# Kernel tuning notes

Measured on AMD Instinct MI355X. Metric: run time of the kernel, lower is better.

The kernel has to match this reference:

```python
import jax, jax.numpy as jnp
import numpy as np

B, T, D = 8, 2048, 256  # batch, time segments, feature dim (a_dim=v_dim=hidden=out=256)
EPS = 1e-8


def _layer_norm(x, g, b, eps=1e-6):
    m = jnp.mean(x, axis=-1, keepdims=True)
    v = jnp.var(x, axis=-1, keepdims=True)
    return (x - m) * jax.lax.rsqrt(v + eps) * g + b


def setup_inputs() -> dict:
    key = jax.random.key(0)
    ks = jax.random.split(key, 9)
    xav = lambda k: jax.random.uniform(k, (D, D), jnp.float32, -1.0, 1.0) * np.sqrt(6.0 / (D + D))
    return {
        "a_fea": jax.random.normal(ks[0], (B, T, D), jnp.float32),
        "v_fea": jax.random.normal(ks[1], (B, T, D), jnp.float32),
        "thr_val": jnp.float32(0.099),
        "Wv1": xav(ks[2]), "Wv2": xav(ks[3]), "Wvfc": xav(ks[4]),
        "Wa1": xav(ks[5]), "Wa2": xav(ks[6]), "Wafc": xav(ks[7]),
        "ln_g": jnp.ones((D,), jnp.float32),
        "ln_b": jnp.zeros((D,), jnp.float32),
    }


def reference(a_fea, v_fea, thr_val, Wv1, Wv2, Wvfc, Wa1, Wa2, Wafc, ln_g, ln_b):
    relu = jax.nn.relu
    # branch projections (dropout is identity at eval); torch Linear: x @ W.T
    v1 = relu(jnp.einsum('btd,hd->bth', v_fea, Wv1))
    v2 = relu(jnp.einsum('btd,hd->bth', v_fea, Wv2))
    a1 = relu(jnp.einsum('btd,hd->bth', a_fea, Wa1))
    a2 = relu(jnp.einsum('btd,hd->bth', a_fea, Wa2))

    d = v2.shape[-1]
    # scaled cross-modal scores, ReLU'd  [B, Tv, Ta]
    beta_va = relu(jnp.einsum('btd,bsd->bts', v2, a1) / jnp.sqrt(jnp.float32(d)))
    # a->v scores taken BEFORE row-normalization of beta_va (as in torch code)
    beta_av = jnp.transpose(beta_va, (0, 2, 1))

    time = beta_va.shape[-1]
    thr = thr_val * 10.0 / time

    # normalize -> threshold sparsify -> renormalize (v attends to a)
    bn_va = beta_va / (jnp.sum(beta_va, axis=-1, keepdims=True) + EPS)
    g_va = jnp.where(bn_va > thr, bn_va, 0.0)
    g_va = g_va / (jnp.sum(g_va, axis=-1, keepdims=True) + EPS)

    # same for a attends to v
    bn_av = beta_av / (jnp.sum(beta_av, axis=-1, keepdims=True) + EPS)
    g_av = jnp.where(bn_av > thr, bn_av, 0.0)
    g_av = g_av / (jnp.sum(g_av, axis=-1, keepdims=True) + EPS)

    # vectorized form of the diagonal selection double-loop (batch element 0)
    pred = (jnp.diagonal(g_av[0]) > 0).astype(jnp.float32)  # [T]

    a_pos = jnp.einsum('bts,bsd->btd', g_va, a2)
    v_psp = v_fea + a_pos
    v_pos = jnp.einsum('bts,bsd->btd', g_av, v1)
    a_psp = a_fea + v_pos

    v_psp = _layer_norm(relu(jnp.einsum('btd,od->bto', v_psp, Wvfc)), ln_g, ln_b)
    a_psp = _layer_norm(relu(jnp.einsum('btd,od->bto', a_psp, Wafc)), ln_g, ln_b)
    a_v_fuse = 0.5 * (v_psp + a_psp)
    return a_v_fuse, v_psp, a_psp, pred
```

## Files before the change

### kernel.cpp

```cpp
#include <hip/hip_runtime.h>
#include <math.h>

#define TT 2048
#define DD 256
#define NBATCH 8
#define EPSF 1e-8f

typedef unsigned short u16;
typedef __attribute__((ext_vector_type(8))) short short8;
typedef __attribute__((ext_vector_type(4))) float f32x4;

__device__ __forceinline__ u16 f2bf(float x) {
    unsigned int u = __builtin_bit_cast(unsigned int, x);
    u += 0x7fffu + ((u >> 16) & 1u);
    return (u16)(u >> 16);
}
__device__ __forceinline__ float bf2f(u16 h) {
    return __builtin_bit_cast(float, (unsigned int)h << 16);
}

__device__ __forceinline__ int frag_dst(int row, int k) {
    return (((row >> 4) * 4 + (k >> 3)) * 16 + (row & 15)) * 8 + (k & 7);
}

__device__ __forceinline__ int swz(int i) { return i ^ ((i >> 2) & 32); }

template<int BR>
__device__ __forceinline__ void stage_tile(const u16* __restrict__ g, u16* s,
                                           int row0, int k0, int ldk, int tid)
{
    #pragma unroll
    for (int i = 0; i < BR / 64; ++i) {
        const int c = tid + 256 * i;
        const int row = c >> 2, q = c & 3;
        *(int4*)(s + swz(frag_dst(row, q * 8))) =
            *(const int4*)(g + (long)(row0 + row) * ldk + k0 + q * 8);
    }
}

__global__ __launch_bounds__(512)
void proj_kernel(const u16* __restrict__ vfh, const u16* __restrict__ vfl,
                 const u16* __restrict__ afh, const u16* __restrict__ afl,
                 const u16* __restrict__ Wsp,
                 u16* __restrict__ v2h, u16* __restrict__ v2l,
                 u16* __restrict__ a1h, u16* __restrict__ a1l,
                 u16* __restrict__ v1T, u16* __restrict__ a2T)
{
    const int zz = blockIdx.z;
    const u16* Ah = (zz == 1 || zz == 3) ? afh : vfh;
    const u16* Al = (zz == 1 || zz == 3) ? afl : vfl;
    const int widx = (zz == 0) ? 2 : (zz == 1) ? 4 : (zz == 2) ? 0 : 6;
    const u16* Bh = Wsp + widx * DD * DD;
    const u16* Bl = Bh + DD * DD;
    const bool split = zz < 2;
    u16* Oh = (zz == 0) ? v2h : a1h;
    u16* Ol = (zz == 0) ? v2l : a1l;
    u16* OT = (zz == 2) ? v1T : a2T;

    __shared__ __align__(16) u16 Ah_s[128 * 32], Al_s[128 * 32];
    __shared__ __align__(16) u16 Bh_s[64 * 32], Bl_s[64 * 32];
    const int m0 = blockIdx.y * 128, n0 = blockIdx.x * 64;
    const int tid = threadIdx.x, lane = tid & 63, w = tid >> 6;
    const int wy = w >> 2, wx = w & 3;
    f32x4 acc[4] = {};

    const int prow = tid >> 2, pq = tid & 3;
    const int dA = swz(frag_dst(prow, pq * 8));
    const u16* gAh = Ah + (long)(m0 + prow) * DD + pq * 8;
    const u16* gAl = Al + (long)(m0 + prow) * DD + pq * 8;
    const int brow = (tid & 255) >> 2, bq = tid & 3;
    const int dB = swz(frag_dst(brow, bq * 8));
    const u16* gB = ((tid < 256) ? Bh : Bl) + (long)(n0 + brow) * DD + bq * 8;
    u16* sB = (tid < 256) ? Bh_s : Bl_s;

    int4 rAh = *(const int4*)(gAh);
    int4 rAl = *(const int4*)(gAl);
    int4 rB  = *(const int4*)(gB);

    for (int k0 = 0; k0 < DD; k0 += 32) {
        *(int4*)(Ah_s + dA) = rAh;
        *(int4*)(Al_s + dA) = rAl;
        *(int4*)(sB + dB)   = rB;
        __syncthreads();
        const int kn = (k0 + 32 < DD) ? k0 + 32 : 0;
        rAh = *(const int4*)(gAh + kn);
        rAl = *(const int4*)(gAl + kn);
        rB  = *(const int4*)(gB + kn);
        short8 ah[4], al[4], bh, bl;
        #pragma unroll
        for (int i = 0; i < 4; ++i) {
            ah[i] = *(const short8*)(Ah_s + swz(((wy * 4 + i) * 64 + lane) * 8));
            al[i] = *(const short8*)(Al_s + swz(((wy * 4 + i) * 64 + lane) * 8));
        }
        bh = *(const short8*)(Bh_s + swz((wx * 64 + lane) * 8));
        bl = *(const short8*)(Bl_s + swz((wx * 64 + lane) * 8));
        #pragma unroll
        for (int i = 0; i < 4; ++i) {
            acc[i] = __builtin_amdgcn_mfma_f32_16x16x32_bf16(ah[i], bl, acc[i], 0, 0, 0);
            acc[i] = __builtin_amdgcn_mfma_f32_16x16x32_bf16(al[i], bh, acc[i], 0, 0, 0);
            acc[i] = __builtin_amdgcn_mfma_f32_16x16x32_bf16(ah[i], bh, acc[i], 0, 0, 0);
        }
        __syncthreads();
    }
    const int quad = lane >> 4, col = lane & 15;
    const int c = n0 + wx * 16 + col;
    #pragma unroll
    for (int i = 0; i < 4; ++i) {
        const int rbase = m0 + wy * 64 + i * 16 + quad * 4;
        if (split) {
            #pragma unroll
            for (int r = 0; r < 4; ++r) {
                const float v = fmaxf(acc[i][r], 0.f);
                const u16 h = f2bf(v);
                Oh[(long)(rbase + r) * DD + c] = h;
                Ol[(long)(rbase + r) * DD + c] = f2bf(v - bf2f(h));
            }
        } else {
            short4 pk;
            pk.x = (short)f2bf(fmaxf(acc[i][0], 0.f));
            pk.y = (short)f2bf(fmaxf(acc[i][1], 0.f));
            pk.z = (short)f2bf(fmaxf(acc[i][2], 0.f));
            pk.w = (short)f2bf(fmaxf(acc[i][3], 0.f));
            const int b = rbase >> 11, t = rbase & (TT - 1);
            *(short4*)(OT + ((long)b * DD + c) * TT + t) = pk;
        }
    }
}

__global__ __launch_bounds__(512)
void score_kernel(const u16* __restrict__ v2h, const u16* __restrict__ v2l,
                  const u16* __restrict__ a1h, const u16* __restrict__ a1l,
                  u16* __restrict__ beta, u16* __restrict__ betaT,
                  float* __restrict__ rs, float* __restrict__ cs)
{
    __shared__ __align__(16) u16 S[128 * 136];
    u16* Ah_s = S;
    u16* Al_s = S + 4096;
    u16* Bh_s = S + 8192;
    u16* Bl_s = S + 12288;
    const int z = blockIdx.z;
    const int m0 = blockIdx.y * 128, n0 = blockIdx.x * 128;
    const int tid = threadIdx.x, lane = tid & 63, w = tid >> 6;
    const int wy = w >> 2, wx = w & 3;
    const long zoff = (long)z * TT * DD;
    f32x4 acc[4][2] = {};

    const int prow = tid >> 2, pq = tid & 3;
    const int d0 = swz(frag_dst(prow, pq * 8));
    const u16* gAh = v2h + zoff + (long)(m0 + prow) * DD + pq * 8;
    const u16* gAl = v2l + zoff + (long)(m0 + prow) * DD + pq * 8;
    const u16* gBh = a1h + zoff + (long)(n0 + prow) * DD + pq * 8;
    const u16* gBl = a1l + zoff + (long)(n0 + prow) * DD + pq * 8;

    int4 rAh = *(const int4*)(gAh);
    int4 rAl = *(const int4*)(gAl);
    int4 rBh = *(const int4*)(gBh);
    int4 rBl = *(const int4*)(gBl);

    for (int k0 = 0; k0 < DD; k0 += 32) {
        *(int4*)(Ah_s + d0) = rAh;
        *(int4*)(Al_s + d0) = rAl;
        *(int4*)(Bh_s + d0) = rBh;
        *(int4*)(Bl_s + d0) = rBl;
        __syncthreads();
        const int kn = (k0 + 32 < DD) ? k0 + 32 : 0;
        rAh = *(const int4*)(gAh + kn);
        rAl = *(const int4*)(gAl + kn);
        rBh = *(const int4*)(gBh + kn);
        rBl = *(const int4*)(gBl + kn);
        short8 ah[4], al[4], bh[2], bl[2];
        #pragma unroll
        for (int i = 0; i < 4; ++i) {
            ah[i] = *(const short8*)(Ah_s + swz(((wy * 4 + i) * 64 + lane) * 8));
            al[i] = *(const short8*)(Al_s + swz(((wy * 4 + i) * 64 + lane) * 8));
        }
        #pragma unroll
        for (int j = 0; j < 2; ++j) {
            bh[j] = *(const short8*)(Bh_s + swz(((wx * 2 + j) * 64 + lane) * 8));
            bl[j] = *(const short8*)(Bl_s + swz(((wx * 2 + j) * 64 + lane) * 8));
        }
        #pragma unroll
        for (int i = 0; i < 4; ++i)
            #pragma unroll
            for (int j = 0; j < 2; ++j) {
                acc[i][j] = __builtin_amdgcn_mfma_f32_16x16x32_bf16(ah[i], bl[j], acc[i][j], 0, 0, 0);
                acc[i][j] = __builtin_amdgcn_mfma_f32_16x16x32_bf16(al[i], bh[j], acc[i][j], 0, 0, 0);
                acc[i][j] = __builtin_amdgcn_mfma_f32_16x16x32_bf16(ah[i], bh[j], acc[i][j], 0, 0, 0);
            }
        __syncthreads();
    }

    const int quad = lane >> 4, col = lane & 15;
    const float scale = 1.f / 16.f;
    #pragma unroll
    for (int i = 0; i < 4; ++i)
        #pragma unroll
        for (int j = 0; j < 2; ++j)
            #pragma unroll
            for (int r = 0; r < 4; ++r)
                acc[i][j][r] = fmaxf(acc[i][j][r] * scale, 0.f);

    #pragma unroll
    for (int i = 0; i < 4; ++i) {
        const int rl = (wy * 4 + i) * 16 + quad * 4;
        #pragma unroll
        for (int j = 0; j < 2; ++j) {
            const int cl = (wx * 2 + j) * 16 + col;
            #pragma unroll
            for (int r = 0; r < 4; ++r)
                S[(rl + r) * 136 + cl] = f2bf(acc[i][j][r]);
        }
    }
    __syncthreads();
    #pragma unroll
    for (int it = 0; it < 4; ++it) {
        const int idx = tid + 512 * it;
        const int rl = idx >> 4, cq = idx & 15;
        const int4 v = *(const int4*)(S + rl * 136 + cq * 8);
        *(int4*)(beta + ((long)z * TT + m0 + rl) * TT + n0 + cq * 8) = v;
    }
    #pragma unroll
    for (int i = 0; i < 4; ++i)
        #pragma unroll
        for (int r = 0; r < 4; ++r) {
            float rp = acc[i][0][r] + acc[i][1][r];
            rp += __shfl_xor(rp, 1); rp += __shfl_xor(rp, 2);
            rp += __shfl_xor(rp, 4); rp += __shfl_xor(rp, 8);
            if (col == 0) {
                const int row = m0 + (wy * 4 + i) * 16 + quad * 4 + r;
                atomicAdd(&rs[(long)z * TT + row], rp);
            }
        }
    #pragma unroll
    for (int j = 0; j < 2; ++j) {
        float cp = 0.f;
        #pragma unroll
        for (int i = 0; i < 4; ++i)
            #pragma unroll
            for (int r = 0; r < 4; ++r) cp += acc[i][j][r];
        cp += __shfl_xor(cp, 16); cp += __shfl_xor(cp, 32);
        if (lane < 16) {
            const int c = n0 + (wx * 2 + j) * 16 + col;
            atomicAdd(&cs[(long)z * TT + c], cp);
        }
    }
    __syncthreads();
    #pragma unroll
    for (int i = 0; i < 4; ++i)
        #pragma unroll
        for (int j = 0; j < 2; ++j) {
            const int cl = (wx * 2 + j) * 16 + col;
            const int rl = (wy * 4 + i) * 16 + quad * 4;
            short4 pk;
            pk.x = (short)f2bf(acc[i][j][0]);
            pk.y = (short)f2bf(acc[i][j][1]);
            pk.z = (short)f2bf(acc[i][j][2]);
            pk.w = (short)f2bf(acc[i][j][3]);
            *(short4*)(S + cl * 136 + rl) = pk;
        }
    __syncthreads();
    #pragma unroll
    for (int it = 0; it < 4; ++it) {
        const int idx = tid + 512 * it;
        const int cl = idx >> 4, tq = idx & 15;
        const int4 v = *(const int4*)(S + cl * 136 + tq * 8);
        *(int4*)(betaT + ((long)z * TT + n0 + cl) * TT + m0 + tq * 8) = v;
    }
}

__global__ __launch_bounds__(512)
void pv_kernel(const u16* __restrict__ beta, const u16* __restrict__ betaT,
               const u16* __restrict__ a2T, const u16* __restrict__ v1T,
               const float* __restrict__ rs, const float* __restrict__ cs,
               const float* __restrict__ thrp,
               const float* __restrict__ v_fea, const float* __restrict__ a_fea,
               u16* __restrict__ yvin, u16* __restrict__ yain)
{
    __shared__ __align__(16) u16 A_s[128 * 32], B_s[256 * 32];
    __shared__ float sthr[128], sA[128], ssum[128];
    const int zz = blockIdx.x;
    const int m0 = blockIdx.y * 128;
    const int z = zz & 7;
    const bool av = zz >= 8;
    const u16* P      = av ? betaT : beta;
    const u16* VT     = av ? v1T : a2T;
    const float* sums = av ? cs : rs;
    const float* resid = av ? a_fea : v_fea;
    u16* outb         = av ? yain : yvin;

    const int tid = threadIdx.x, lane = tid & 63, w = tid >> 6;
    const int wy = w >> 2, wx = w & 3;
    const float thr = thrp[0] * 10.0f / (float)TT;
    if (tid < 128) {
        const float s = sums[(long)z * TT + m0 + tid];
        sA[tid] = s; sthr[tid] = thr * (s + EPSF); ssum[tid] = 0.f;
    }
    __syncthreads();
    f32x4 acc[4][4] = {};
    float rpart = 0.f;
    const int arow = tid >> 2, aq = tid & 3;
    const u16* Pp = P + ((long)z * TT + m0 + arow) * TT + aq * 8;
    const u16* V0 = VT + (long)z * DD * TT + (long)arow * TT + aq * 8;
    const u16* V1 = V0 + (long)128 * TT;
    const int da  = swz(frag_dst(arow, aq * 8));
    const int db1 = swz(frag_dst(arow + 128, aq * 8));

    int4 Ar  = *(const int4*)(Pp);
    int4 Br0 = *(const int4*)(V0);
    int4 Br1 = *(const int4*)(V1);

    for (int k0 = 0; k0 < TT; k0 += 32) {
        union { int4 v; u16 us[8]; } U;
        U.v = Ar;
        const float ct = sthr[arow];
        float ss = 0.f;
        #pragma unroll
        for (int t = 0; t < 8; ++t) {
            const float v = bf2f(U.us[t]);
            if (v > ct) ss += v; else U.us[t] = 0;
        }
        rpart += ss;
        *(int4*)(A_s + da) = U.v;
        *(int4*)(B_s + da) = Br0;
        *(int4*)(B_s + db1) = Br1;
        __syncthreads();
        const int kn = (k0 + 32 < TT) ? (k0 + 32) : k0;
        Ar  = *(const int4*)(Pp + kn);
        Br0 = *(const int4*)(V0 + kn);
        Br1 = *(const int4*)(V1 + kn);
        short8 a[4], b[4];
        #pragma unroll
        for (int i = 0; i < 4; ++i)
            a[i] = *(const short8*)(A_s + swz(((wy * 4 + i) * 64 + lane) * 8));
        #pragma unroll
        for (int j = 0; j < 4; ++j)
            b[j] = *(const short8*)(B_s + swz(((wx * 4 + j) * 64 + lane) * 8));
        #pragma unroll
        for (int i = 0; i < 4; ++i)
            #pragma unroll
            for (int j = 0; j < 4; ++j)
                acc[i][j] = __builtin_amdgcn_mfma_f32_16x16x32_bf16(a[i], b[j], acc[i][j], 0, 0, 0);
        __syncthreads();
    }
    atomicAdd(&ssum[arow], rpart);
    __syncthreads();

    const int quad = lane >> 4, col = lane & 15;
    #pragma unroll
    for (int i = 0; i < 4; ++i)
        #pragma unroll
        for (int j = 0; j < 4; ++j) {
            const int c = (wx * 4 + j) * 16 + col;
            #pragma unroll
            for (int r = 0; r < 4; ++r) {
                const int lrow = (wy * 4 + i) * 16 + quad * 4 + r;
                const int row = m0 + lrow;
                const float inv = 1.0f / (ssum[lrow] + EPSF * (sA[lrow] + EPSF));
                const float v = acc[i][j][r] * inv + resid[((long)z * TT + row) * DD + c];
                outb[((long)z * TT + row) * DD + c] = f2bf(v);
            }
        }
}

__global__ __launch_bounds__(512)
void fc_kernel(const u16* __restrict__ Ain, const u16* __restrict__ Wb,
               u16* __restrict__ Cb)
{
    const int z = blockIdx.z;
    const u16* A = Ain + (size_t)z * (size_t)NBATCH * TT * DD;
    const u16* B = Wb + (size_t)z * DD * DD;
    u16* C = Cb + (size_t)z * (size_t)NBATCH * TT * DD;
    __shared__ __align__(16) u16 A_s[128 * 32], B_s[64 * 32];
    const int m0 = blockIdx.y * 128, n0 = blockIdx.x * 64;
    const int tid = threadIdx.x, lane = tid & 63, w = tid >> 6;
    const int wy = w >> 2, wx = w & 3;
    f32x4 acc[4] = {};

    const int prow = tid >> 2, pq = tid & 3;
    const int dA = swz(frag_dst(prow, pq * 8));
    const u16* gA = A + (long)(m0 + prow) * DD + pq * 8;
    const int brow = (tid & 255) >> 2, bq = tid & 3;
    const int dB = swz(frag_dst(brow, bq * 8));
    const u16* gB = B + (long)(n0 + brow) * DD + bq * 8;

    int4 rA = *(const int4*)(gA);
    int4 rB = *(const int4*)(gB);

    for (int k0 = 0; k0 < DD; k0 += 32) {
        *(int4*)(A_s + dA) = rA;
        if (tid < 256) *(int4*)(B_s + dB) = rB;
        __syncthreads();
        const int kn = (k0 + 32 < DD) ? k0 + 32 : 0;
        rA = *(const int4*)(gA + kn);
        rB = *(const int4*)(gB + kn);
        short8 a[4], b;
        #pragma unroll
        for (int i = 0; i < 4; ++i)
            a[i] = *(const short8*)(A_s + swz(((wy * 4 + i) * 64 + lane) * 8));
        b = *(const short8*)(B_s + swz((wx * 64 + lane) * 8));
        #pragma unroll
        for (int i = 0; i < 4; ++i)
            acc[i] = __builtin_amdgcn_mfma_f32_16x16x32_bf16(a[i], b, acc[i], 0, 0, 0);
        __syncthreads();
    }
    const int quad = lane >> 4, col = lane & 15;
    const int c = n0 + wx * 16 + col;
    #pragma unroll
    for (int i = 0; i < 4; ++i) {
        #pragma unroll
        for (int r = 0; r < 4; ++r) {
            const int row = m0 + wy * 64 + i * 16 + quad * 4 + r;
            C[(long)row * DD + c] = f2bf(fmaxf(acc[i][r], 0.f));
        }
    }
}

__global__ __launch_bounds__(256)
void pred_exact(const float* __restrict__ vf, const float* __restrict__ af,
                const float* __restrict__ Wv2, const float* __restrict__ Wa1,
                const float* __restrict__ cs, const float* __restrict__ thrp,
                float* __restrict__ pred)
{
    __shared__ float vs[8][260];
    __shared__ float as_[8][260];
    __shared__ float red[4][8];
    const int t0 = blockIdx.x * 8;
    const int tid = threadIdx.x;
    {
        const int i = tid >> 5, c = (tid & 31) * 8;
        *(float4*)&vs[i][c] = *(const float4*)(vf + (long)(t0 + i) * DD + c);
        *(float4*)&vs[i][c + 4] = *(const float4*)(vf + (long)(t0 + i) * DD + c + 4);
        *(float4*)&as_[i][c] = *(const float4*)(af + (long)(t0 + i) * DD + c);
        *(float4*)&as_[i][c + 4] = *(const float4*)(af + (long)(t0 + i) * DD + c + 4);
    }
    __syncthreads();
    const int j = tid;
    float av[8] = {0.f}, aa[8] = {0.f};
    for (int k = 0; k < DD; k += 4) {
        const float4 wv = *(const float4*)(Wv2 + (long)j * DD + k);
        const float4 wa = *(const float4*)(Wa1 + (long)j * DD + k);
        #pragma unroll
        for (int i = 0; i < 8; ++i) {
            const float4 x = *(const float4*)&vs[i][k];
            av[i] += wv.x * x.x + wv.y * x.y + wv.z * x.z + wv.w * x.w;
            const float4 y = *(const float4*)&as_[i][k];
            aa[i] += wa.x * y.x + wa.y * y.y + wa.z * y.z + wa.w * y.w;
        }
    }
    float p[8];
    #pragma unroll
    for (int i = 0; i < 8; ++i)
        p[i] = fmaxf(av[i], 0.f) * fmaxf(aa[i], 0.f);
    #pragma unroll
    for (int off = 32; off > 0; off >>= 1)
        #pragma unroll
        for (int i = 0; i < 8; ++i) p[i] += __shfl_xor(p[i], off);
    const int lane = tid & 63, wv_ = tid >> 6;
    if (lane == 0)
        #pragma unroll
        for (int i = 0; i < 8; ++i) red[wv_][i] = p[i];
    __syncthreads();
    if (tid < 8) {
        float d = red[0][tid] + red[1][tid] + red[2][tid] + red[3][tid];
        d = fmaxf(d * (1.f / 16.f), 0.f);
        const float thr = thrp[0] * 10.0f / (float)TT;
        pred[t0 + tid] = (d > thr * (cs[t0 + tid] + EPSF)) ? 1.0f : 0.0f;
    }
}

__global__ __launch_bounds__(256)
void split_feat(const float* __restrict__ vf, const float* __restrict__ af,
                u16* __restrict__ vfh, u16* __restrict__ vfl,
                u16* __restrict__ afh, u16* __restrict__ afl)
{
    const long i4 = ((long)blockIdx.x * 256 + threadIdx.x) * 4;
    const float* src = blockIdx.y ? af : vf;
    u16* dh = blockIdx.y ? afh : vfh;
    u16* dl = blockIdx.y ? afl : vfl;
    float4 a = *(const float4*)(src + i4);
    ushort4 h4, l4; u16 h;
    h = f2bf(a.x); h4.x = h; l4.x = f2bf(a.x - bf2f(h));
    h = f2bf(a.y); h4.y = h; l4.y = f2bf(a.y - bf2f(h));
    h = f2bf(a.z); h4.z = h; l4.z = f2bf(a.z - bf2f(h));
    h = f2bf(a.w); h4.w = h; l4.w = f2bf(a.w - bf2f(h));
    *(ushort4*)(dh + i4) = h4;
    *(ushort4*)(dl + i4) = l4;
}

__global__ __launch_bounds__(256)
void split_w(const float* __restrict__ w0, const float* __restrict__ w1,
             const float* __restrict__ w2, const float* __restrict__ w3,
             const float* __restrict__ w4, const float* __restrict__ w5,
             u16* __restrict__ out)
{
    const int t = blockIdx.y;
    const float* w = (t == 0) ? w0 : (t == 1) ? w1 : (t == 2) ? w2
                   : (t == 3) ? w3 : (t == 4) ? w4 : w5;
    const int i4 = (blockIdx.x * 256 + threadIdx.x) * 4;
    float4 a = *(const float4*)(w + i4);
    if (t < 4) {
        u16* oh = out + (size_t)t * 2 * DD * DD;
        u16* ol = oh + DD * DD;
        ushort4 h4, l4; u16 h;
        h = f2bf(a.x); h4.x = h; l4.x = f2bf(a.x - bf2f(h));
        h = f2bf(a.y); h4.y = h; l4.y = f2bf(a.y - bf2f(h));
        h = f2bf(a.z); h4.z = h; l4.z = f2bf(a.z - bf2f(h));
        h = f2bf(a.w); h4.w = h; l4.w = f2bf(a.w - bf2f(h));
        *(ushort4*)(oh + i4) = h4;
        *(ushort4*)(ol + i4) = l4;
    } else {
        u16* ob = out + (size_t)8 * DD * DD + (size_t)(t - 4) * DD * DD;
        ushort4 o;
        o.x = f2bf(a.x); o.y = f2bf(a.y); o.z = f2bf(a.z); o.w = f2bf(a.w);
        *(ushort4*)(ob + i4) = o;
    }
}

__global__ __launch_bounds__(256)
void ln_fuse_kernel(const u16* __restrict__ yv, const u16* __restrict__ ya,
                    const float* __restrict__ g, const float* __restrict__ b,
                    float* __restrict__ fuse, float* __restrict__ vpsp,
                    float* __restrict__ apsp)
{
    const long row = (long)blockIdx.x * 4 + (threadIdx.x >> 6);
    const int lane = threadIdx.x & 63;
    const ushort4 hv = *(const ushort4*)(yv + row * DD + lane * 4);
    const ushort4 ha = *(const ushort4*)(ya + row * DD + lane * 4);
    const float xv0 = bf2f(hv.x), xv1 = bf2f(hv.y), xv2 = bf2f(hv.z), xv3 = bf2f(hv.w);
    const float xa0 = bf2f(ha.x), xa1 = bf2f(ha.y), xa2 = bf2f(ha.z), xa3 = bf2f(ha.w);
    float sv = xv0 + xv1 + xv2 + xv3;
    float sa = xa0 + xa1 + xa2 + xa3;
    #pragma unroll
    for (int off = 32; off > 0; off >>= 1) {
        sv += __shfl_xor(sv, off);
        sa += __shfl_xor(sa, off);
    }
    const float mv = sv * (1.f / 256.f);
    const float ma = sa * (1.f / 256.f);
    const float dv0 = xv0 - mv, dv1 = xv1 - mv, dv2 = xv2 - mv, dv3 = xv3 - mv;
    const float da0 = xa0 - ma, da1 = xa1 - ma, da2 = xa2 - ma, da3 = xa3 - ma;
    float qv = dv0 * dv0 + dv1 * dv1 + dv2 * dv2 + dv3 * dv3;
    float qa = da0 * da0 + da1 * da1 + da2 * da2 + da3 * da3;
    #pragma unroll
    for (int off = 32; off > 0; off >>= 1) {
        qv += __shfl_xor(qv, off);
        qa += __shfl_xor(qa, off);
    }
    const float rv = rsqrtf(qv * (1.f / 256.f) + 1e-6f);
    const float ra = rsqrtf(qa * (1.f / 256.f) + 1e-6f);
    const float4 gg = *(const float4*)(g + lane * 4);
    const float4 bb = *(const float4*)(b + lane * 4);
    float4 ov, oa, of;
    ov.x = dv0 * rv * gg.x + bb.x; ov.y = dv1 * rv * gg.y + bb.y;
    ov.z = dv2 * rv * gg.z + bb.z; ov.w = dv3 * rv * gg.w + bb.w;
    oa.x = da0 * ra * gg.x + bb.x; oa.y = da1 * ra * gg.y + bb.y;
    oa.z = da2 * ra * gg.z + bb.z; oa.w = da3 * ra * gg.w + bb.w;
    of.x = 0.5f * (ov.x + oa.x); of.y = 0.5f * (ov.y + oa.y);
    of.z = 0.5f * (ov.z + oa.z); of.w = 0.5f * (ov.w + oa.w);
    *(float4*)(vpsp + row * DD + lane * 4) = ov;
    *(float4*)(apsp + row * DD + lane * 4) = oa;
    *(float4*)(fuse + row * DD + lane * 4) = of;
}

extern "C" void kernel_launch(void* const* d_in, const int* in_sizes, int n_in,
                              void* d_out, int out_size, void* d_ws, size_t ws_size,
                              hipStream_t stream)
{
    const float* a_fea = (const float*)d_in[0];
    const float* v_fea = (const float*)d_in[1];
    const float* thrp  = (const float*)d_in[2];
    const float* Wv1   = (const float*)d_in[3];
    const float* Wv2   = (const float*)d_in[4];
    const float* Wvfc  = (const float*)d_in[5];
    const float* Wa1   = (const float*)d_in[6];
    const float* Wa2   = (const float*)d_in[7];
    const float* Wafc  = (const float*)d_in[8];
    const float* lng   = (const float*)d_in[9];
    const float* lnb   = (const float*)d_in[10];

    const long MT = (long)NBATCH * TT;
    float* out_fuse = (float*)d_out;
    float* out_vpsp = out_fuse + MT * DD;
    float* out_apsp = out_vpsp + MT * DD;
    float* out_pred = out_apsp + MT * DD;

    char* ws = (char*)d_ws;
    const size_t fb = (size_t)MT * DD * sizeof(u16);
    const size_t sumB = (size_t)MT * sizeof(float);
    u16* v2h  = (u16*)(ws + 0 * fb);
    u16* v2l  = (u16*)(ws + 1 * fb);
    u16* a1h  = (u16*)(ws + 2 * fb);
    u16* a1l  = (u16*)(ws + 3 * fb);
    u16* yvin = (u16*)(ws + 4 * fb);
    u16* yain = (u16*)(ws + 5 * fb);
    u16* v1T  = (u16*)(ws + 6 * fb);
    u16* a2T  = (u16*)(ws + 7 * fb);
    char* p = ws + 8 * fb;
    float* rs = (float*)(p + 0 * sumB);
    float* cs = (float*)(p + 1 * sumB);
    u16* Wsp  = (u16*)(p + 2 * sumB);
    char* q = p + 2 * sumB + 10 * DD * DD * sizeof(u16);
    const size_t betaB = (size_t)NBATCH * TT * TT * sizeof(u16);
    u16* beta  = (u16*)q;
    u16* betaT = (u16*)(q + betaB);
    u16* vfh = (u16*)q;
    u16* vfl = vfh + MT * DD;
    u16* afh = vfl + MT * DD;
    u16* afl = afh + MT * DD;
    u16* yvb = (u16*)(ws + 0 * fb);
    u16* yab = yvb + (size_t)MT * DD;

    hipMemsetAsync(rs, 0, 2 * sumB, stream);

    const dim3 blk(256, 1, 1);

    split_feat<<<dim3((unsigned)(MT * DD / 1024), 2, 1), blk, 0, stream>>>(
        v_fea, a_fea, vfh, vfl, afh, afl);
    split_w<<<dim3(DD * DD / 1024, 6, 1), blk, 0, stream>>>(
        Wv1, Wv2, Wa1, Wa2, Wvfc, Wafc, Wsp);

    proj_kernel<<<dim3(DD / 64, (unsigned)(MT / 128), 4), dim3(512, 1, 1), 0, stream>>>(
        vfh, vfl, afh, afl, Wsp, v2h, v2l, a1h, a1l, v1T, a2T);

    score_kernel<<<dim3(TT / 128, TT / 128, NBATCH), dim3(512, 1, 1), 0, stream>>>(
        v2h, v2l, a1h, a1l, beta, betaT, rs, cs);
    pred_exact<<<dim3(TT / 8, 1, 1), blk, 0, stream>>>(
        v_fea, a_fea, Wv2, Wa1, cs, thrp, out_pred);

    pv_kernel<<<dim3(2 * NBATCH, TT / 128, 1), dim3(512, 1, 1), 0, stream>>>(
        beta, betaT, a2T, v1T, rs, cs, thrp, v_fea, a_fea, yvin, yain);

    fc_kernel<<<dim3(DD / 64, (unsigned)(MT / 128), 2), dim3(512, 1, 1), 0, stream>>>(
        yvin, Wsp + 8 * DD * DD, yvb);
    ln_fuse_kernel<<<dim3((unsigned)(MT / 4), 1, 1), blk, 0, stream>>>(
        yvb, yab, lng, lnb, out_fuse, out_vpsp, out_apsp);
}
```

Baseline: 400.6 us.

## Double-buffer shared memory in score and PV kernels with two-deep register prefetch

Both the score GEMM and the PV GEMM now use two shared-memory buffers and two sets of prefetch registers, so staging the next tile overlaps the MFMA work on the current tile and only one barrier is needed per step instead of two. The score kernel's K loop is fully unrolled by hand into eight stages. This cuts barrier stalls and hides global-load latency, at the cost of twice the LDS footprint and more registers, which may lower occupancy.

```diff
diff --git a/kernel.cpp b/kernel.cpp
--- a/kernel.cpp
+++ b/kernel.cpp
@@ -133,11 +133,9 @@
                   u16* __restrict__ beta, u16* __restrict__ betaT,
                   float* __restrict__ rs, float* __restrict__ cs)
 {
-    __shared__ __align__(16) u16 S[128 * 136];
-    u16* Ah_s = S;
-    u16* Al_s = S + 4096;
-    u16* Bh_s = S + 8192;
-    u16* Bl_s = S + 12288;
+    __shared__ __align__(16) u16 S[32768];
+    u16* L0 = S;
+    u16* L1 = S + 16384;
     const int z = blockIdx.z;
     const int m0 = blockIdx.y * 128, n0 = blockIdx.x * 128;
     const int tid = threadIdx.x, lane = tid & 63, w = tid >> 6;
@@ -152,32 +150,34 @@
     const u16* gBh = a1h + zoff + (long)(n0 + prow) * DD + pq * 8;
     const u16* gBl = a1l + zoff + (long)(n0 + prow) * DD + pq * 8;
 
-    int4 rAh = *(const int4*)(gAh);
-    int4 rAl = *(const int4*)(gAl);
-    int4 rBh = *(const int4*)(gBh);
-    int4 rBl = *(const int4*)(gBl);
-
-    for (int k0 = 0; k0 < DD; k0 += 32) {
-        *(int4*)(Ah_s + d0) = rAh;
-        *(int4*)(Al_s + d0) = rAl;
-        *(int4*)(Bh_s + d0) = rBh;
-        *(int4*)(Bl_s + d0) = rBl;
-        __syncthreads();
-        const int kn = (k0 + 32 < DD) ? k0 + 32 : 0;
-        rAh = *(const int4*)(gAh + kn);
-        rAl = *(const int4*)(gAl + kn);
-        rBh = *(const int4*)(gBh + kn);
-        rBl = *(const int4*)(gBl + kn);
+    int4 rA0h, rA0l, rB0h, rB0l, rA1h, rA1l, rB1h, rB1l;
+    auto refill0 = [&](int k) {
+        rA0h = *(const int4*)(gAh + k); rA0l = *(const int4*)(gAl + k);
+        rB0h = *(const int4*)(gBh + k); rB0l = *(const int4*)(gBl + k);
+    };
+    auto refill1 = [&](int k) {
+        rA1h = *(const int4*)(gAh + k); rA1l = *(const int4*)(gAl + k);
+        rB1h = *(const int4*)(gBh + k); rB1l = *(const int4*)(gBl + k);
+    };
+    auto stage0 = [&](u16* L) {
+        *(int4*)(L + d0) = rA0h;         *(int4*)(L + 4096 + d0) = rA0l;
+        *(int4*)(L + 8192 + d0) = rB0h;  *(int4*)(L + 12288 + d0) = rB0l;
+    };
+    auto stage1 = [&](u16* L) {
+        *(int4*)(L + d0) = rA1h;         *(int4*)(L + 4096 + d0) = rA1l;
+        *(int4*)(L + 8192 + d0) = rB1h;  *(int4*)(L + 12288 + d0) = rB1l;
+    };
+    auto compute = [&](const u16* L) {
         short8 ah[4], al[4], bh[2], bl[2];
         #pragma unroll
         for (int i = 0; i < 4; ++i) {
-            ah[i] = *(const short8*)(Ah_s + swz(((wy * 4 + i) * 64 + lane) * 8));
-            al[i] = *(const short8*)(Al_s + swz(((wy * 4 + i) * 64 + lane) * 8));
+            ah[i] = *(const short8*)(L + swz(((wy * 4 + i) * 64 + lane) * 8));
+            al[i] = *(const short8*)(L + 4096 + swz(((wy * 4 + i) * 64 + lane) * 8));
         }
         #pragma unroll
         for (int j = 0; j < 2; ++j) {
-            bh[j] = *(const short8*)(Bh_s + swz(((wx * 2 + j) * 64 + lane) * 8));
-            bl[j] = *(const short8*)(Bl_s + swz(((wx * 2 + j) * 64 + lane) * 8));
+            bh[j] = *(const short8*)(L + 8192 + swz(((wx * 2 + j) * 64 + lane) * 8));
+            bl[j] = *(const short8*)(L + 12288 + swz(((wx * 2 + j) * 64 + lane) * 8));
         }
         #pragma unroll
         for (int i = 0; i < 4; ++i)
@@ -187,8 +187,19 @@
                 acc[i][j] = __builtin_amdgcn_mfma_f32_16x16x32_bf16(al[i], bh[j], acc[i][j], 0, 0, 0);
                 acc[i][j] = __builtin_amdgcn_mfma_f32_16x16x32_bf16(ah[i], bh[j], acc[i][j], 0, 0, 0);
             }
-        __syncthreads();
-    }
+    };
+
+    refill0(0); refill1(32);
+    stage0(L0); refill0(64);
+    __syncthreads();
+    stage1(L1); refill1(96);  compute(L0); __syncthreads();
+    stage0(L0); refill0(128); compute(L1); __syncthreads();
+    stage1(L1); refill1(160); compute(L0); __syncthreads();
+    stage0(L0); refill0(192); compute(L1); __syncthreads();
+    stage1(L1); refill1(224); compute(L0); __syncthreads();
+    stage0(L0);               compute(L1); __syncthreads();
+    stage1(L1);               compute(L0); __syncthreads();
+                              compute(L1); __syncthreads();
 
     const int quad = lane >> 4, col = lane & 15;
     const float scale = 1.f / 16.f;
@@ -276,8 +287,10 @@
                const float* __restrict__ v_fea, const float* __restrict__ a_fea,
                u16* __restrict__ yvin, u16* __restrict__ yain)
 {
-    __shared__ __align__(16) u16 A_s[128 * 32], B_s[256 * 32];
+    __shared__ __align__(16) u16 PS[24576];
     __shared__ float sthr[128], sA[128], ssum[128];
+    u16* L0 = PS;
+    u16* L1 = PS + 12288;
     const int zz = blockIdx.x;
     const int m0 = blockIdx.y * 128;
     const int z = zz & 7;
@@ -305,41 +318,58 @@
     const int da  = swz(frag_dst(arow, aq * 8));
     const int db1 = swz(frag_dst(arow + 128, aq * 8));
 
-    int4 Ar  = *(const int4*)(Pp);
-    int4 Br0 = *(const int4*)(V0);
-    int4 Br1 = *(const int4*)(V1);
-
-    for (int k0 = 0; k0 < TT; k0 += 32) {
+    int4 A0, B00, B10, A1, B01, B11;
+    auto refill0 = [&](int k) {
+        A0 = *(const int4*)(Pp + k); B00 = *(const int4*)(V0 + k); B10 = *(const int4*)(V1 + k);
+    };
+    auto refill1 = [&](int k) {
+        A1 = *(const int4*)(Pp + k); B01 = *(const int4*)(V0 + k); B11 = *(const int4*)(V1 + k);
+    };
+    auto stageP = [&](u16* L, const int4& vA, const int4& vB0, const int4& vB1) {
         union { int4 v; u16 us[8]; } U;
-        U.v = Ar;
-        const float ct = sthr[arow];
+        U.v = vA;
+        const float cthr = sthr[arow];
         float ss = 0.f;
         #pragma unroll
         for (int t = 0; t < 8; ++t) {
             const float v = bf2f(U.us[t]);
-            if (v > ct) ss += v; else U.us[t] = 0;
+            if (v > cthr) ss += v; else U.us[t] = 0;
         }
         rpart += ss;
-        *(int4*)(A_s + da) = U.v;
-        *(int4*)(B_s + da) = Br0;
-        *(int4*)(B_s + db1) = Br1;
-        __syncthreads();
-        const int kn = (k0 + 32 < TT) ? (k0 + 32) : k0;
-        Ar  = *(const int4*)(Pp + kn);
-        Br0 = *(const int4*)(V0 + kn);
-        Br1 = *(const int4*)(V1 + kn);
+        *(int4*)(L + da) = U.v;
+        *(int4*)(L + 4096 + da) = vB0;
+        *(int4*)(L + 4096 + db1) = vB1;
+    };
+    auto computeP = [&](const u16* L) {
         short8 a[4], b[4];
         #pragma unroll
         for (int i = 0; i < 4; ++i)
-            a[i] = *(const short8*)(A_s + swz(((wy * 4 + i) * 64 + lane) * 8));
+            a[i] = *(const short8*)(L + swz(((wy * 4 + i) * 64 + lane) * 8));
         #pragma unroll
         for (int j = 0; j < 4; ++j)
-            b[j] = *(const short8*)(B_s + swz(((wx * 4 + j) * 64 + lane) * 8));
+            b[j] = *(const short8*)(L + 4096 + swz(((wx * 4 + j) * 64 + lane) * 8));
         #pragma unroll
         for (int i = 0; i < 4; ++i)
             #pragma unroll
             for (int j = 0; j < 4; ++j)
                 acc[i][j] = __builtin_amdgcn_mfma_f32_16x16x32_bf16(a[i], b[j], acc[i][j], 0, 0, 0);
+    };
+
+    refill0(0); refill1(32);
+    stageP(L0, A0, B00, B10);
+    refill0(64);
+    __syncthreads();
+
+    for (int k0 = 0; k0 < TT; k0 += 64) {
+        stageP(L1, A1, B01, B11);
+        refill1((k0 + 96 < TT) ? k0 + 96 : 0);
+        computeP(L0);
+        __syncthreads();
+        if (k0 + 64 < TT) {
+            stageP(L0, A0, B00, B10);
+            refill0((k0 + 128 < TT) ? k0 + 128 : 0);
+        }
+        computeP(L1);
         __syncthreads();
     }
     atomicAdd(&ssum[arow], rpart);
```

Result: faster. 371.4 us (-7.3%).
